# Optimization experiments

Hardware: AMD Instinct MI355X
Metric: run time of the kernel (lower is better)

## Reference

```python
import jax, jax.numpy as jnp
import numpy as np
import math

WP, WF = 10, 10      # past/future window
EPS = 1e-8           # torch cosine_similarity eps
CLIP = 1.0 - 1e-6    # keep arccos (and its grad) finite
MAXN = 110           # hard-coded alpha width in the module


def setup_inputs() -> dict:
    key = jax.random.key(0)
    k1, k2, k3, k4, k5, k6 = jax.random.split(key, 6)
    B, L, G, N, D = 32, 110, 512, 40, 300
    node_features = jax.random.normal(k1, (B, L, G), jnp.float32)
    knowledge = jax.random.normal(k2, (B, L, N, D), jnp.float32)
    anew = jax.random.uniform(k3, (B, L, N), jnp.float32)
    var_sem = 2.0 / (G + G)
    var_con = 2.0 / (D + D)
    weight_sem = jax.random.normal(k4, (G, G), jnp.float32) * var_sem
    weight_con = jax.random.normal(k5, (D, D), jnp.float32) * var_con
    text_len = jax.random.randint(k6, (B,), 55, L + 1, jnp.int32)
    return dict(node_features=node_features, knowledge=knowledge, anew=anew,
                weight_sem=weight_sem, weight_con=weight_con, text_len=text_len)


def reference(node_features, knowledge, anew, weight_sem, weight_con, text_len):
    B, L, G = node_features.shape
    N = knowledge.shape[2]
    dt = node_features.dtype

    # window + validity mask, replaces per-(i,j) python slicing: [B, j, k]
    j = jnp.arange(L)[:, None]
    k = jnp.arange(L)[None, :]
    cur = text_len[:, None, None]
    mask = (k >= j - WP) & (k <= j + WF)
    mask = mask[None] & (k[None, :, :] <= cur - 1) & (j[None, :, :] < cur)
    fmask = mask.astype(dt)

    # ---- semantic branch: score = 1 - acos(cos_sim(f_j, W_sem f_k))/pi, windowed softmax
    att_sem = jnp.einsum('st,blt->bls', weight_sem, node_features)      # [B,L,G]
    num = jnp.einsum('bjg,bkg->bjk', node_features, att_sem)
    nf = jnp.maximum(jnp.linalg.norm(node_features, axis=-1), EPS)      # [B,L]
    na = jnp.maximum(jnp.linalg.norm(att_sem, axis=-1), EPS)            # [B,L]
    cos = num / (nf[:, :, None] * na[:, None, :])
    score = 1.0 - jnp.arccos(jnp.clip(cos, -CLIP, CLIP)) / math.pi
    neg = jnp.finfo(dt).min
    s = jnp.where(mask, score, neg)
    s = s - jnp.max(s, axis=-1, keepdims=True)
    e = jnp.exp(s) * fmask
    alphas_sem = e / jnp.maximum(jnp.sum(e, axis=-1, keepdims=True), EPS)  # [B,L,L]

    # ---- affinity transform of anew: v -> (||[v, v/2] - [0.5, 0]|| - 0.06467)/0.607468
    anew_aff = (jnp.sqrt((anew - 0.5) ** 2 + (0.5 * anew) ** 2) - 0.06467) / 0.607468

    # ---- contextual branch: windowed sum_n |cos_sim(aff_feat_{k,n}, knowledge_{j,n})|
    att_con = jnp.einsum('blns,st->blnt', knowledge, weight_con)        # [B,L,N,D]
    aff_feat = att_con * anew_aff[..., None]                            # [B,L,N,D]
    num_c = jnp.einsum('bknd,bjnd->bjkn', aff_feat, knowledge)          # [B,j,k,N]
    n_f = jnp.maximum(jnp.linalg.norm(aff_feat, axis=-1), EPS)          # [B,k,N]
    n_k = jnp.maximum(jnp.linalg.norm(knowledge, axis=-1), EPS)         # [B,j,N]
    cos_c = num_c / (n_f[:, None, :, :] * n_k[:, :, None, :])
    alphas_con = 10.0 * jnp.sum(jnp.abs(cos_c), axis=-1) * fmask        # [B,j,k]

    out = 0.5 * alphas_sem + 0.5 * alphas_con                           # [B,L,L]
    if L < MAXN:  # module hard-codes width 110
        out = jnp.pad(out, ((0, 0), (0, 0), (0, MAXN - L)))
    return out
```

## Files before the change

kernel.cpp:

```cpp
#include <hip/hip_runtime.h>
#include <hip/hip_bf16.h>
#include <math.h>

constexpr int Bb   = 32;
constexpr int Ls   = 110;
constexpr int Gs   = 512;
constexpr int Ns   = 40;
constexpr int Ds   = 300;
constexpr int WPc  = 10;
constexpr int WFc  = 10;
constexpr int MAXNc = 110;
constexpr float EPSf  = 1e-8f;
constexpr float CLIPf = 1.0f - 1e-6f;
constexpr int BL = Bb * Ls;
constexpr int Mrows = BL * Ns;
constexpr int BPITCH = 328;
constexpr int RGRP = Mrows / 256;

typedef __attribute__((ext_vector_type(8))) short short8_t;
typedef __attribute__((ext_vector_type(4))) short short4_t;
typedef __attribute__((ext_vector_type(4))) float floatx4;

__device__ __forceinline__ unsigned short bf16r(float f) {
  unsigned u = __float_as_uint(f);
  u += 0x7fffu + ((u >> 16) & 1u);
  return (unsigned short)(u >> 16);
}

__device__ __forceinline__ unsigned pkbf(float lo, float hi) {
  unsigned a = __float_as_uint(lo), b = __float_as_uint(hi);
  a += 0x7fffu + ((a >> 16) & 1u);
  b += 0x7fffu + ((b >> 16) & 1u);
  return (a >> 16) | (b & 0xffff0000u);
}

__device__ __forceinline__ short8_t cvt8(const float4 v0, const float4 v1) {
  union { short8_t s; unsigned u[4]; } p;
  p.u[0] = pkbf(v0.x, v0.y);
  p.u[1] = pkbf(v0.z, v0.w);
  p.u[2] = pkbf(v1.x, v1.y);
  p.u[3] = pkbf(v1.z, v1.w);
  return p.s;
}

__global__ __launch_bounds__(256) void transpose_wsem(const float* __restrict__ w,
                                                      float* __restrict__ wt) {
  __shared__ float tile[32][33];
  const int bx = blockIdx.x * 32;
  const int by = blockIdx.y * 32;
  const int tx = threadIdx.x;
  const int ty = threadIdx.y;
#pragma unroll
  for (int r = ty; r < 32; r += 8)
    tile[r][tx] = w[(by + r) * Gs + (bx + tx)];
  __syncthreads();
#pragma unroll
  for (int r = ty; r < 32; r += 8)
    wt[(bx + r) * Gs + (by + tx)] = tile[tx][r];
}

__global__ __launch_bounds__(256) void wct_prep(const float* __restrict__ wc,
                                                short* __restrict__ wct) {
  __shared__ float tile[32][33];
  const int t0 = blockIdx.x * 32;
  const int s0 = blockIdx.y * 32;
  const int tx = threadIdx.x, ty = threadIdx.y;
#pragma unroll
  for (int r = ty; r < 32; r += 8) {
    const int s = s0 + r, t = t0 + tx;
    tile[r][tx] = (s < Ds && t < Ds) ? wc[s * Ds + t] : 0.f;
  }
  __syncthreads();
#pragma unroll
  for (int r = ty; r < 32; r += 8) {
    const int t = t0 + r, s = s0 + tx;
    wct[t * 320 + s] = (short)bf16r(tile[tx][r]);
  }
}

__global__ __launch_bounds__(512) void sem_gemm(const float* __restrict__ nf,
                                                const float* __restrict__ wt,
                                                float* __restrict__ att_sem,
                                                float* __restrict__ na_arr) {
  const int bl0 = blockIdx.x * 8;
  const int s = threadIdx.x;
  const float* __restrict__ x0 = nf + (size_t)bl0 * Gs;
  float acc[8];
#pragma unroll
  for (int r = 0; r < 8; ++r) acc[r] = 0.f;
#pragma unroll 4
  for (int t = 0; t < Gs; ++t) {
    const float wv = wt[t * Gs + s];
#pragma unroll
    for (int r = 0; r < 8; ++r) acc[r] = fmaf(wv, x0[r * Gs + t], acc[r]);
  }
#pragma unroll
  for (int r = 0; r < 8; ++r) att_sem[(size_t)(bl0 + r) * Gs + s] = acc[r];

  __shared__ float partial[8][8];
  const int wave = s >> 6, lane = s & 63;
#pragma unroll
  for (int r = 0; r < 8; ++r) {
    float v = acc[r] * acc[r];
#pragma unroll
    for (int off = 32; off > 0; off >>= 1) v += __shfl_xor(v, off);
    if (lane == 0) partial[r][wave] = v;
  }
  __syncthreads();
  if (s < 8) {
    float sum = 0.f;
#pragma unroll
    for (int w2 = 0; w2 < 8; ++w2) sum += partial[s][w2];
    na_arr[bl0 + s] = fmaxf(sqrtf(sum), EPSf);
  }
}

__global__ __launch_bounds__(256) void sem_attn(const float* __restrict__ nf,
                                                const float* __restrict__ att_sem,
                                                const float* __restrict__ na_arr,
                                                const int* __restrict__ tlen,
                                                float* __restrict__ out) {
  const int blk = blockIdx.x;
  const int b = blk / Ls, j = blk % Ls;
  const int len = tlen[b];
  float* __restrict__ orow = out + (size_t)(b * Ls + j) * MAXNc;
  if (j >= len) {
    for (int k = threadIdx.x; k < MAXNc; k += 256) orow[k] = 0.f;
    return;
  }
  const int k0 = max(j - WPc, 0);
  const int k1 = min(j + WFc, len - 1);
  const int nk = k1 - k0 + 1;

  __shared__ float xs[Gs];
  __shared__ float sc[21];
  __shared__ float red[4];

  const float* __restrict__ x = nf + (size_t)(b * Ls + j) * Gs;
  float ss = 0.f;
  for (int t = threadIdx.x; t < Gs; t += 256) {
    const float v = x[t];
    xs[t] = v;
    ss += v * v;
  }
  const int wave = threadIdx.x >> 6, lane = threadIdx.x & 63;
#pragma unroll
  for (int off = 32; off > 0; off >>= 1) ss += __shfl_xor(ss, off);
  if (lane == 0) red[wave] = ss;
  __syncthreads();
  const float nfn = fmaxf(sqrtf(red[0] + red[1] + red[2] + red[3]), EPSf);

  for (int i = wave; i < nk; i += 4) {
    const int k = k0 + i;
    const float* __restrict__ as = att_sem + (size_t)(b * Ls + k) * Gs;
    float d = 0.f;
#pragma unroll
    for (int t = lane; t < Gs; t += 64) d = fmaf(xs[t], as[t], d);
#pragma unroll
    for (int off = 32; off > 0; off >>= 1) d += __shfl_xor(d, off);
    if (lane == 0) {
      float cs = d / (nfn * na_arr[b * Ls + k]);
      cs = fminf(fmaxf(cs, -CLIPf), CLIPf);
      sc[i] = 1.0f - acosf(cs) * (float)(1.0 / M_PI);
    }
  }
  __syncthreads();
  if (threadIdx.x == 0) {
    float m = -1e30f;
    for (int i = 0; i < nk; ++i) m = fmaxf(m, sc[i]);
    red[0] = m;
  }
  __syncthreads();
  const float m = red[0];
  if ((int)threadIdx.x < nk) sc[threadIdx.x] = expf(sc[threadIdx.x] - m);
  __syncthreads();
  if (threadIdx.x == 0) {
    float s = 0.f;
    for (int i = 0; i < nk; ++i) s += sc[i];
    red[1] = 1.0f / fmaxf(s, EPSf);
  }
  __syncthreads();
  const float inv = red[1];
  for (int k = threadIdx.x; k < MAXNc; k += 256) {
    float v = 0.f;
    if (k >= k0 && k <= k1) v = 0.5f * sc[k - k0] * inv;
    orow[k] = v;
  }
}

__global__ __launch_bounds__(256, 3) void con_gemm_mfma(const float* __restrict__ kn,
                                                        const short* __restrict__ wct,
                                                        const int* __restrict__ tlen,
                                                        unsigned short* __restrict__ ybar,
                                                        float* __restrict__ rowss) {
  const int lin = blockIdx.x;
  const int xcd = lin & 7, slot = lin >> 3;
  const int m = slot & 3;
  const int g = xcd + 8 * (slot >> 2);
  if (g >= RGRP) return;
  const int rowbase = g * 256;
  const int n0 = m * 80;

  __shared__ short Bl[80 * BPITCH];
  const int tid = threadIdx.x;
  for (int s = tid; s < 80 * 40; s += 256) {
    const int nl = s / 40, sl = s % 40;
    *reinterpret_cast<short8_t*>(&Bl[nl * BPITCH + sl * 8]) =
        *reinterpret_cast<const short8_t*>(wct + (n0 + nl) * 320 + sl * 8);
  }
  __syncthreads();

  const int wave = tid >> 6, lane = tid & 63;
  const int quad = lane >> 4, l16 = lane & 15;

#pragma unroll
  for (int tt = 0; tt < 4; ++tt) {
    const int row0 = rowbase + wave * 64 + tt * 16;
    const int blA = row0 / Ns, blB = (row0 + 15) / Ns;
    const bool alive = ((blA % Ls) < tlen[blA / Ls]) | ((blB % Ls) < tlen[blB / Ls]);
    if (!alive) continue;

    const float* __restrict__ arow = kn + (size_t)(row0 + l16) * Ds;

    float4 A0[4], A1[4];
#pragma unroll
    for (int p = 0; p < 4; ++p) {
      const int d0 = p * 32 + quad * 8;
      A0[p] = *reinterpret_cast<const float4*>(arow + d0);
      A1[p] = *reinterpret_cast<const float4*>(arow + d0 + 4);
    }

    floatx4 acc[5];
#pragma unroll
    for (int i = 0; i < 5; ++i) acc[i] = (floatx4){0.f, 0.f, 0.f, 0.f};

#pragma unroll
    for (int c = 0; c < 10; ++c) {
      const short8_t afrag = cvt8(A0[c & 3], A1[c & 3]);
      const int pc = c + 4;
      if (pc < 9) {
        const int d0 = pc * 32 + quad * 8;
        A0[c & 3] = *reinterpret_cast<const float4*>(arow + d0);
        A1[c & 3] = *reinterpret_cast<const float4*>(arow + d0 + 4);
      } else if (pc == 9) {
        const int d0 = 288 + quad * 8;
        float4 v0 = make_float4(0.f, 0.f, 0.f, 0.f);
        float4 v1 = make_float4(0.f, 0.f, 0.f, 0.f);
        if (quad == 0) {
          v0 = *reinterpret_cast<const float4*>(arow + d0);
          v1 = *reinterpret_cast<const float4*>(arow + d0 + 4);
        } else if (quad == 1) {
          v0 = *reinterpret_cast<const float4*>(arow + d0);
        }
        A0[c & 3] = v0;
        A1[c & 3] = v1;
      }
#pragma unroll
      for (int i = 0; i < 5; ++i) {
        const short8_t bfrag = *reinterpret_cast<const short8_t*>(
            &Bl[(i * 16 + l16) * BPITCH + c * 32 + quad * 8]);
        acc[i] = __builtin_amdgcn_mfma_f32_16x16x32_bf16(afrag, bfrag, acc[i], 0, 0, 0);
      }
    }

#pragma unroll
    for (int r = 0; r < 4; ++r) {
      float p = 0.f;
#pragma unroll
      for (int i = 0; i < 5; ++i) p = fmaf(acc[i][r], acc[i][r], p);
      p += __shfl_xor(p, 1);
      p += __shfl_xor(p, 2);
      p += __shfl_xor(p, 4);
      p += __shfl_xor(p, 8);
      if (l16 == 0) atomicAdd(&rowss[row0 + quad * 4 + r], p);
    }
#pragma unroll
    for (int i = 0; i < 5; ++i) {
      const int col = n0 + i * 16 + l16;
      if (col < Ds) {
#pragma unroll
        for (int r = 0; r < 4; ++r)
          ybar[(size_t)(row0 + quad * 4 + r) * Ds + col] = bf16r(acc[i][r]);
      }
    }
  }
}

__global__ __launch_bounds__(512) void con_attn_mfma(const float* __restrict__ kn,
                                                     const unsigned short* __restrict__ ybar,
                                                     const float* __restrict__ rowss,
                                                     const float* __restrict__ anew,
                                                     const int* __restrict__ tlen,
                                                     float* __restrict__ out) {
  const int b = blockIdx.x / 7;
  const int jt = blockIdx.x % 7;
  const int j0 = jt * 16;
  const int len = tlen[b];
  if (j0 >= len) return;
  const int kbase = min(max(j0 - WPc, 0), Ls - 48);

  const int tid = threadIdx.x;
  const int wave = tid >> 6, lane = tid & 63;
  const int quad = lane >> 4, l16 = lane & 15;

  __shared__ float red[8][768];

  const int jj = min(j0 + l16, Ls - 1);
  const size_t blj = (size_t)(b * Ls + jj);

  float outacc[3][4];
#pragma unroll
  for (int t = 0; t < 3; ++t)
#pragma unroll
    for (int r = 0; r < 4; ++r) outacc[t][r] = 0.f;

  const unsigned short* yrow[3];
  int krow_m[3];
#pragma unroll
  for (int t = 0; t < 3; ++t) {
    const int k = kbase + t * 16 + l16;
    yrow[t] = ybar + ((size_t)(b * Ls + k) * Ns) * Ds;
    krow_m[t] = (b * Ls + k) * Ns;
  }

  for (int ni = 0; ni < 5; ++ni) {
    const int n = wave + ni * 8;
    const float* __restrict__ arow = kn + (blj * Ns + n) * Ds;

    float w_t[3];
#pragma unroll
    for (int t = 0; t < 3; ++t) {
      const int mm = krow_m[t] + n;
      const float a = anew[mm];
      const float ssqk = rowss[mm];
      const float aff = (sqrtf((a - 0.5f) * (a - 0.5f) + 0.25f * a * a) - 0.06467f) *
                        (1.0f / 0.607468f);
      w_t[t] = aff / fmaxf(aff * sqrtf(ssqk), EPSf);
    }

    floatx4 S[3];
#pragma unroll
    for (int t = 0; t < 3; ++t) S[t] = (floatx4){0.f, 0.f, 0.f, 0.f};
    float ssq = 0.f;

#pragma unroll
    for (int c = 0; c < 10; ++c) {
      const int d0 = c * 32 + quad * 8;
      float av[8];
      if (c < 9) {
        const float4 v0 = *reinterpret_cast<const float4*>(arow + d0);
        const float4 v1 = *reinterpret_cast<const float4*>(arow + d0 + 4);
        av[0] = v0.x; av[1] = v0.y; av[2] = v0.z; av[3] = v0.w;
        av[4] = v1.x; av[5] = v1.y; av[6] = v1.z; av[7] = v1.w;
      } else {
        if (quad == 0) {
          const float4 v0 = *reinterpret_cast<const float4*>(arow + d0);
          const float4 v1 = *reinterpret_cast<const float4*>(arow + d0 + 4);
          av[0] = v0.x; av[1] = v0.y; av[2] = v0.z; av[3] = v0.w;
          av[4] = v1.x; av[5] = v1.y; av[6] = v1.z; av[7] = v1.w;
        } else if (quad == 1) {
          const float4 v0 = *reinterpret_cast<const float4*>(arow + d0);
          av[0] = v0.x; av[1] = v0.y; av[2] = v0.z; av[3] = v0.w;
          av[4] = av[5] = av[6] = av[7] = 0.f;
        } else {
#pragma unroll
          for (int e = 0; e < 8; ++e) av[e] = 0.f;
        }
      }
      short8_t afrag;
#pragma unroll
      for (int e = 0; e < 8; ++e) {
        ssq = fmaf(av[e], av[e], ssq);
        afrag[e] = (short)bf16r(av[e]);
      }
#pragma unroll
      for (int t = 0; t < 3; ++t) {
        const unsigned short* yr = yrow[t] + (size_t)n * Ds;
        short8_t bfrag;
        if (c < 9) {
          const short4_t u0 = *reinterpret_cast<const short4_t*>(yr + d0);
          const short4_t u1 = *reinterpret_cast<const short4_t*>(yr + d0 + 4);
          bfrag[0] = u0.x; bfrag[1] = u0.y; bfrag[2] = u0.z; bfrag[3] = u0.w;
          bfrag[4] = u1.x; bfrag[5] = u1.y; bfrag[6] = u1.z; bfrag[7] = u1.w;
        } else {
          if (quad == 0) {
            const short4_t u0 = *reinterpret_cast<const short4_t*>(yr + d0);
            const short4_t u1 = *reinterpret_cast<const short4_t*>(yr + d0 + 4);
            bfrag[0] = u0.x; bfrag[1] = u0.y; bfrag[2] = u0.z; bfrag[3] = u0.w;
            bfrag[4] = u1.x; bfrag[5] = u1.y; bfrag[6] = u1.z; bfrag[7] = u1.w;
          } else if (quad == 1) {
            const short4_t u0 = *reinterpret_cast<const short4_t*>(yr + d0);
            bfrag[0] = u0.x; bfrag[1] = u0.y; bfrag[2] = u0.z; bfrag[3] = u0.w;
            bfrag[4] = bfrag[5] = bfrag[6] = bfrag[7] = 0;
          } else {
#pragma unroll
            for (int e = 0; e < 8; ++e) bfrag[e] = 0;
          }
        }
        S[t] = __builtin_amdgcn_mfma_f32_16x16x32_bf16(afrag, bfrag, S[t], 0, 0, 0);
      }
    }

    ssq += __shfl_xor(ssq, 16);
    ssq += __shfl_xor(ssq, 32);
    const float kinv = 1.0f / fmaxf(sqrtf(ssq), EPSf);

#pragma unroll
    for (int r = 0; r < 4; ++r) {
      const float kv = __shfl(kinv, quad * 4 + r);
#pragma unroll
      for (int t = 0; t < 3; ++t)
        outacc[t][r] = fmaf(kv * w_t[t], fabsf(S[t][r]), outacc[t][r]);
    }
  }

#pragma unroll
  for (int t = 0; t < 3; ++t)
#pragma unroll
    for (int r = 0; r < 4; ++r)
      red[wave][(quad * 4 + r) * 48 + t * 16 + l16] = outacc[t][r];
  __syncthreads();

  for (int idx = tid; idx < 768; idx += 512) {
    float s = 0.f;
#pragma unroll
    for (int w = 0; w < 8; ++w) s += red[w][idx];
    const int j = j0 + idx / 48;
    const int k = kbase + idx % 48;
    if (j < len && k < len && k >= j - WPc && k <= j + WFc)
      out[(size_t)(b * Ls + j) * MAXNc + k] += 5.0f * s;
  }
}

extern "C" void kernel_launch(void* const* d_in, const int* in_sizes, int n_in,
                              void* d_out, int out_size, void* d_ws, size_t ws_size,
                              hipStream_t stream) {
  const float* nf   = (const float*)d_in[0];
  const float* kn   = (const float*)d_in[1];
  const float* anew = (const float*)d_in[2];
  const float* wsem = (const float*)d_in[3];
  const float* wcon = (const float*)d_in[4];
  const int*   tlen = (const int*)d_in[5];
  float* out = (float*)d_out;

  float* att_sem = (float*)d_ws;
  float* na_arr  = att_sem + (size_t)BL * Gs;
  float* wt      = na_arr + BL;
  short* wct     = (short*)(wt + (size_t)Gs * Gs);
  float* rowss   = (float*)(wct + 320 * 320);
  unsigned short* ybar = (unsigned short*)(rowss + Mrows);

  hipMemsetAsync(rowss, 0, (size_t)Mrows * sizeof(float), stream);
  transpose_wsem<<<dim3(16, 16), dim3(32, 8), 0, stream>>>(wsem, wt);
  wct_prep<<<dim3(10, 10), dim3(32, 8), 0, stream>>>(wcon, wct);
  sem_gemm<<<BL / 8, 512, 0, stream>>>(nf, wt, att_sem, na_arr);
  sem_attn<<<BL, 256, 0, stream>>>(nf, att_sem, na_arr, tlen, out);
  con_gemm_mfma<<<2208, 256, 0, stream>>>(kn, wct, tlen, ybar, rowss);
  con_attn_mfma<<<Bb * 7, 512, 0, stream>>>(kn, ybar, rowss, anew, tlen, out);
}
```

Measured before the change: 497.1 us.

## Precompute bf16 padded knowledge and row norms; batch four row tiles per wave in GEMM

Adds a kn_prep kernel that converts the knowledge tensor once to bf16 with a 320-element row pitch and stores per-row inverse norms. The contextual GEMM and attention kernels then read these aligned bf16 rows directly, dropping in-loop fp32-to-bf16 conversion, the ragged tail handling and the on-the-fly norm accumulation. The GEMM is also restructured so each wave keeps four 16-row tiles in flight and reuses each LDS B fragment across them. The cost is an extra full pass over knowledge, including rows past text_len that were previously skipped, plus an extra workspace buffer and more accumulator registers per wave.

```diff
diff --git a/kernel.cpp b/kernel.cpp
--- a/kernel.cpp
+++ b/kernel.cpp
@@ -15,6 +15,7 @@
 constexpr int BL = Bb * Ls;
 constexpr int Mrows = BL * Ns;
 constexpr int BPITCH = 328;
+constexpr int KST = 320;
 constexpr int RGRP = Mrows / 256;
 
 typedef __attribute__((ext_vector_type(8))) short short8_t;
@@ -74,7 +75,34 @@
 #pragma unroll
   for (int r = ty; r < 32; r += 8) {
     const int t = t0 + r, s = s0 + tx;
-    wct[t * 320 + s] = (short)bf16r(tile[tx][r]);
+    wct[t * KST + s] = (short)bf16r(tile[tx][r]);
+  }
+}
+
+__global__ __launch_bounds__(256) void kn_prep(const float* __restrict__ kn,
+                                               unsigned short* __restrict__ knb,
+                                               float* __restrict__ kninv) {
+  const int wid = (blockIdx.x * 256 + threadIdx.x) >> 6;
+  const int lane = threadIdx.x & 63;
+  const int nwaves = gridDim.x * 4;
+  for (int row = wid; row < Mrows; row += nwaves) {
+    const float* __restrict__ src = kn + (size_t)row * Ds;
+    float4 v0 = make_float4(0.f, 0.f, 0.f, 0.f);
+    float4 v1 = v0;
+    const int d0 = lane * 8;
+    if (lane < 37) {
+      v0 = *reinterpret_cast<const float4*>(src + d0);
+      v1 = *reinterpret_cast<const float4*>(src + d0 + 4);
+    } else if (lane == 37) {
+      v0 = *reinterpret_cast<const float4*>(src + d0);
+    }
+    float ss = v0.x * v0.x + v0.y * v0.y + v0.z * v0.z + v0.w * v0.w +
+               v1.x * v1.x + v1.y * v1.y + v1.z * v1.z + v1.w * v1.w;
+#pragma unroll
+    for (int off = 32; off > 0; off >>= 1) ss += __shfl_xor(ss, off);
+    if (lane < 40)
+      *reinterpret_cast<short8_t*>(knb + (size_t)row * KST + d0) = cvt8(v0, v1);
+    if (lane == 0) kninv[row] = 1.0f / fmaxf(sqrtf(ss), EPSf);
   }
 }
 
@@ -188,7 +216,7 @@
   }
 }
 
-__global__ __launch_bounds__(256, 3) void con_gemm_mfma(const float* __restrict__ kn,
+__global__ __launch_bounds__(256, 3) void con_gemm_mfma(const unsigned short* __restrict__ knb,
                                                         const short* __restrict__ wct,
                                                         const int* __restrict__ tlen,
                                                         unsigned short* __restrict__ ybar,
@@ -206,68 +234,69 @@
   for (int s = tid; s < 80 * 40; s += 256) {
     const int nl = s / 40, sl = s % 40;
     *reinterpret_cast<short8_t*>(&Bl[nl * BPITCH + sl * 8]) =
-        *reinterpret_cast<const short8_t*>(wct + (n0 + nl) * 320 + sl * 8);
+        *reinterpret_cast<const short8_t*>(wct + (n0 + nl) * KST + sl * 8);
   }
   __syncthreads();
 
   const int wave = tid >> 6, lane = tid & 63;
   const int quad = lane >> 4, l16 = lane & 15;
-
+  const int wrow = rowbase + wave * 64;
+
+  {
+    bool any = false;
+    for (int bl = wrow / Ns; bl <= (wrow + 63) / Ns; ++bl)
+      any |= (bl % Ls) < tlen[bl / Ls];
+    if (!any) return;
+  }
+
+  const unsigned short* arow[4];
+#pragma unroll
+  for (int tt = 0; tt < 4; ++tt)
+    arow[tt] = knb + (size_t)(wrow + tt * 16 + l16) * KST + quad * 8;
+
+  floatx4 acc[4][5];
+#pragma unroll
+  for (int tt = 0; tt < 4; ++tt)
+#pragma unroll
+    for (int i = 0; i < 5; ++i) acc[tt][i] = (floatx4){0.f, 0.f, 0.f, 0.f};
+
+  short8_t A[3][4];
 #pragma unroll
   for (int tt = 0; tt < 4; ++tt) {
-    const int row0 = rowbase + wave * 64 + tt * 16;
+    A[0][tt] = *reinterpret_cast<const short8_t*>(arow[tt]);
+    A[1][tt] = *reinterpret_cast<const short8_t*>(arow[tt] + 32);
+  }
+
+#pragma unroll
+  for (int c = 0; c < 10; ++c) {
+    if (c < 8) {
+#pragma unroll
+      for (int tt = 0; tt < 4; ++tt)
+        A[(c + 2) % 3][tt] =
+            *reinterpret_cast<const short8_t*>(arow[tt] + (c + 2) * 32);
+    }
+#pragma unroll
+    for (int i = 0; i < 5; ++i) {
+      const short8_t bfrag = *reinterpret_cast<const short8_t*>(
+          &Bl[(i * 16 + l16) * BPITCH + c * 32 + quad * 8]);
+#pragma unroll
+      for (int tt = 0; tt < 4; ++tt)
+        acc[tt][i] = __builtin_amdgcn_mfma_f32_16x16x32_bf16(A[c % 3][tt], bfrag,
+                                                             acc[tt][i], 0, 0, 0);
+    }
+  }
+
+#pragma unroll
+  for (int tt = 0; tt < 4; ++tt) {
+    const int row0 = wrow + tt * 16;
     const int blA = row0 / Ns, blB = (row0 + 15) / Ns;
     const bool alive = ((blA % Ls) < tlen[blA / Ls]) | ((blB % Ls) < tlen[blB / Ls]);
     if (!alive) continue;
-
-    const float* __restrict__ arow = kn + (size_t)(row0 + l16) * Ds;
-
-    float4 A0[4], A1[4];
-#pragma unroll
-    for (int p = 0; p < 4; ++p) {
-      const int d0 = p * 32 + quad * 8;
-      A0[p] = *reinterpret_cast<const float4*>(arow + d0);
-      A1[p] = *reinterpret_cast<const float4*>(arow + d0 + 4);
-    }
-
-    floatx4 acc[5];
-#pragma unroll
-    for (int i = 0; i < 5; ++i) acc[i] = (floatx4){0.f, 0.f, 0.f, 0.f};
-
-#pragma unroll
-    for (int c = 0; c < 10; ++c) {
-      const short8_t afrag = cvt8(A0[c & 3], A1[c & 3]);
-      const int pc = c + 4;
-      if (pc < 9) {
-        const int d0 = pc * 32 + quad * 8;
-        A0[c & 3] = *reinterpret_cast<const float4*>(arow + d0);
-        A1[c & 3] = *reinterpret_cast<const float4*>(arow + d0 + 4);
-      } else if (pc == 9) {
-        const int d0 = 288 + quad * 8;
-        float4 v0 = make_float4(0.f, 0.f, 0.f, 0.f);
-        float4 v1 = make_float4(0.f, 0.f, 0.f, 0.f);
-        if (quad == 0) {
-          v0 = *reinterpret_cast<const float4*>(arow + d0);
-          v1 = *reinterpret_cast<const float4*>(arow + d0 + 4);
-        } else if (quad == 1) {
-          v0 = *reinterpret_cast<const float4*>(arow + d0);
-        }
-        A0[c & 3] = v0;
-        A1[c & 3] = v1;
-      }
-#pragma unroll
-      for (int i = 0; i < 5; ++i) {
-        const short8_t bfrag = *reinterpret_cast<const short8_t*>(
-            &Bl[(i * 16 + l16) * BPITCH + c * 32 + quad * 8]);
-        acc[i] = __builtin_amdgcn_mfma_f32_16x16x32_bf16(afrag, bfrag, acc[i], 0, 0, 0);
-      }
-    }
-
 #pragma unroll
     for (int r = 0; r < 4; ++r) {
       float p = 0.f;
 #pragma unroll
-      for (int i = 0; i < 5; ++i) p = fmaf(acc[i][r], acc[i][r], p);
+      for (int i = 0; i < 5; ++i) p = fmaf(acc[tt][i][r], acc[tt][i][r], p);
       p += __shfl_xor(p, 1);
       p += __shfl_xor(p, 2);
       p += __shfl_xor(p, 4);
@@ -277,18 +306,17 @@
 #pragma unroll
     for (int i = 0; i < 5; ++i) {
       const int col = n0 + i * 16 + l16;
-      if (col < Ds) {
-#pragma unroll
-        for (int r = 0; r < 4; ++r)
-          ybar[(size_t)(row0 + quad * 4 + r) * Ds + col] = bf16r(acc[i][r]);
-      }
-    }
-  }
-}
-
-__global__ __launch_bounds__(512) void con_attn_mfma(const float* __restrict__ kn,
+#pragma unroll
+      for (int r = 0; r < 4; ++r)
+        ybar[(size_t)(row0 + quad * 4 + r) * KST + col] = bf16r(acc[tt][i][r]);
+    }
+  }
+}
+
+__global__ __launch_bounds__(512) void con_attn_mfma(const unsigned short* __restrict__ knb,
                                                      const unsigned short* __restrict__ ybar,
                                                      const float* __restrict__ rowss,
+                                                     const float* __restrict__ kninv,
                                                      const float* __restrict__ anew,
                                                      const int* __restrict__ tlen,
                                                      float* __restrict__ out) {
@@ -319,13 +347,14 @@
 #pragma unroll
   for (int t = 0; t < 3; ++t) {
     const int k = kbase + t * 16 + l16;
-    yrow[t] = ybar + ((size_t)(b * Ls + k) * Ns) * Ds;
+    yrow[t] = ybar + (size_t)(b * Ls + k) * Ns * KST;
     krow_m[t] = (b * Ls + k) * Ns;
   }
 
   for (int ni = 0; ni < 5; ++ni) {
     const int n = wave + ni * 8;
-    const float* __restrict__ arow = kn + (blj * Ns + n) * Ds;
+    const unsigned short* __restrict__ arow =
+        knb + ((blj * Ns + n) * (size_t)KST) + quad * 8;
 
     float w_t[3];
 #pragma unroll
@@ -337,73 +366,22 @@
                         (1.0f / 0.607468f);
       w_t[t] = aff / fmaxf(aff * sqrtf(ssqk), EPSf);
     }
+    const float kinv = kninv[blj * Ns + n];
 
     floatx4 S[3];
 #pragma unroll
     for (int t = 0; t < 3; ++t) S[t] = (floatx4){0.f, 0.f, 0.f, 0.f};
-    float ssq = 0.f;
 
 #pragma unroll
     for (int c = 0; c < 10; ++c) {
-      const int d0 = c * 32 + quad * 8;
-      float av[8];
-      if (c < 9) {
-        const float4 v0 = *reinterpret_cast<const float4*>(arow + d0);
-        const float4 v1 = *reinterpret_cast<const float4*>(arow + d0 + 4);
-        av[0] = v0.x; av[1] = v0.y; av[2] = v0.z; av[3] = v0.w;
-        av[4] = v1.x; av[5] = v1.y; av[6] = v1.z; av[7] = v1.w;
-      } else {
-        if (quad == 0) {
-          const float4 v0 = *reinterpret_cast<const float4*>(arow + d0);
-          const float4 v1 = *reinterpret_cast<const float4*>(arow + d0 + 4);
-          av[0] = v0.x; av[1] = v0.y; av[2] = v0.z; av[3] = v0.w;
-          av[4] = v1.x; av[5] = v1.y; av[6] = v1.z; av[7] = v1.w;
-        } else if (quad == 1) {
-          const float4 v0 = *reinterpret_cast<const float4*>(arow + d0);
-          av[0] = v0.x; av[1] = v0.y; av[2] = v0.z; av[3] = v0.w;
-          av[4] = av[5] = av[6] = av[7] = 0.f;
-        } else {
-#pragma unroll
-          for (int e = 0; e < 8; ++e) av[e] = 0.f;
-        }
-      }
-      short8_t afrag;
-#pragma unroll
-      for (int e = 0; e < 8; ++e) {
-        ssq = fmaf(av[e], av[e], ssq);
-        afrag[e] = (short)bf16r(av[e]);
-      }
+      const short8_t afrag = *reinterpret_cast<const short8_t*>(arow + c * 32);
 #pragma unroll
       for (int t = 0; t < 3; ++t) {
-        const unsigned short* yr = yrow[t] + (size_t)n * Ds;
-        short8_t bfrag;
-        if (c < 9) {
-          const short4_t u0 = *reinterpret_cast<const short4_t*>(yr + d0);
-          const short4_t u1 = *reinterpret_cast<const short4_t*>(yr + d0 + 4);
-          bfrag[0] = u0.x; bfrag[1] = u0.y; bfrag[2] = u0.z; bfrag[3] = u0.w;
-          bfrag[4] = u1.x; bfrag[5] = u1.y; bfrag[6] = u1.z; bfrag[7] = u1.w;
-        } else {
-          if (quad == 0) {
-            const short4_t u0 = *reinterpret_cast<const short4_t*>(yr + d0);
-            const short4_t u1 = *reinterpret_cast<const short4_t*>(yr + d0 + 4);
-            bfrag[0] = u0.x; bfrag[1] = u0.y; bfrag[2] = u0.z; bfrag[3] = u0.w;
-            bfrag[4] = u1.x; bfrag[5] = u1.y; bfrag[6] = u1.z; bfrag[7] = u1.w;
-          } else if (quad == 1) {
-            const short4_t u0 = *reinterpret_cast<const short4_t*>(yr + d0);
-            bfrag[0] = u0.x; bfrag[1] = u0.y; bfrag[2] = u0.z; bfrag[3] = u0.w;
-            bfrag[4] = bfrag[5] = bfrag[6] = bfrag[7] = 0;
-          } else {
-#pragma unroll
-            for (int e = 0; e < 8; ++e) bfrag[e] = 0;
-          }
-        }
+        const short8_t bfrag = *reinterpret_cast<const short8_t*>(
+            yrow[t] + (size_t)n * KST + c * 32 + quad * 8);
         S[t] = __builtin_amdgcn_mfma_f32_16x16x32_bf16(afrag, bfrag, S[t], 0, 0, 0);
       }
     }
-
-    ssq += __shfl_xor(ssq, 16);
-    ssq += __shfl_xor(ssq, 32);
-    const float kinv = 1.0f / fmaxf(sqrtf(ssq), EPSf);
 
 #pragma unroll
     for (int r = 0; r < 4; ++r) {
@@ -447,14 +425,17 @@
   float* na_arr  = att_sem + (size_t)BL * Gs;
   float* wt      = na_arr + BL;
   short* wct     = (short*)(wt + (size_t)Gs * Gs);
-  float* rowss   = (float*)(wct + 320 * 320);
-  unsigned short* ybar = (unsigned short*)(rowss + Mrows);
+  float* rowss   = (float*)(wct + KST * KST);
+  float* kninv   = rowss + Mrows;
+  unsigned short* knb  = (unsigned short*)(kninv + Mrows);
+  unsigned short* ybar = knb + (size_t)Mrows * KST;
 
   hipMemsetAsync(rowss, 0, (size_t)Mrows * sizeof(float), stream);
   transpose_wsem<<<dim3(16, 16), dim3(32, 8), 0, stream>>>(wsem, wt);
   wct_prep<<<dim3(10, 10), dim3(32, 8), 0, stream>>>(wcon, wct);
+  kn_prep<<<2048, 256, 0, stream>>>(kn, knb, kninv);
   sem_gemm<<<BL / 8, 512, 0, stream>>>(nf, wt, att_sem, na_arr);
   sem_attn<<<BL, 256, 0, stream>>>(nf, att_sem, na_arr, tlen, out);
-  con_gemm_mfma<<<2208, 256, 0, stream>>>(kn, wct, tlen, ybar, rowss);
-  con_attn_mfma<<<Bb * 7, 512, 0, stream>>>(kn, ybar, rowss, anew, tlen, out);
-}
+  con_gemm_mfma<<<2208, 256, 0, stream>>>(knb, wct, tlen, ybar, rowss);
+  con_attn_mfma<<<Bb * 7, 512, 0, stream>>>(knb, ybar, rowss, kninv, anew, tlen, out);
+}
```

Measured after the change: 482.7 us. 1.03x faster.
